# Kernel tuning notes

Hardware: AMD Instinct MI355X
Metric: run time of the kernel (lower is better)

The kernel has to match this reference:

```python
import jax, jax.numpy as jnp
import numpy as np

B, NC, P, HW, ED = 64, 20, 4, 224, 128  # batch, num_classes, patch, img, embed_dim
LN_EPS = 1e-5


def setup_inputs() -> dict:
    key = jax.random.key(0)
    k0, k1, k2, k3 = jax.random.split(key, 4)
    rgb = jax.random.normal(k0, (B, 3, HW, HW), jnp.float32)
    mask = jax.random.randint(k1, (B, 1, HW, HW), 0, NC).astype(jnp.int32)
    proj_w = jax.random.normal(k2, (ED, 4, P, P), jnp.float32) * 0.05  # OIHW, in=3+1
    proj_b = jnp.zeros((ED,), jnp.float32)
    ln_gamma = jnp.ones((ED,), jnp.float32)
    ln_beta = jnp.zeros((ED,), jnp.float32)
    sem_emb = jax.random.normal(k3, (NC, ED), jnp.float32) * 0.02
    # weights_dict = {3: 2.0, 7: 5.0, 15: 3.0} on top of ones
    class_weights = jnp.ones((NC,), jnp.float32).at[jnp.array([3, 7, 15])].set(
        jnp.array([2.0, 5.0, 3.0], jnp.float32))
    return dict(rgb=rgb, mask=mask, proj_w=proj_w, proj_b=proj_b,
                ln_gamma=ln_gamma, ln_beta=ln_beta, sem_emb=sem_emb,
                class_weights=class_weights)


def reference(rgb, mask, proj_w, proj_b, ln_gamma, ln_beta, sem_emb, class_weights):
    Bsz, _, H, W = rgb.shape
    Hp, Wp = H // P, W // P
    # --- patch conv embed on [rgb ; mask] ---
    x = jnp.concatenate([rgb, mask.astype(rgb.dtype)], axis=1)  # [B,4,H,W]
    pt = jax.lax.conv_general_dilated(
        x, proj_w, window_strides=(P, P), padding='VALID',
        dimension_numbers=('NCHW', 'OIHW', 'NCHW'))  # [B,ED,Hp,Wp]
    pt = pt + proj_b[None, :, None, None]
    pt = pt.reshape(Bsz, ED, Hp * Wp).transpose(0, 2, 1)  # [B,N,ED]
    # --- LayerNorm over embed dim ---
    mu = pt.mean(-1, keepdims=True)
    var = ((pt - mu) ** 2).mean(-1, keepdims=True)
    pt = (pt - mu) / jnp.sqrt(var + LN_EPS) * ln_gamma + ln_beta
    # --- importance-weighted area histogram downsample (no big one-hot) ---
    m = mask[:, 0].astype(jnp.int32)  # [B,H,W]
    patches = m.reshape(Bsz, Hp, P, Wp, P).transpose(0, 1, 3, 2, 4)
    patches = patches.reshape(Bsz, Hp, Wp, P * P)  # [B,Hp,Wp,16] pixel labels per patch
    # per-patch class counts; fixed small loop over NC classes
    counts = jnp.stack([(patches == c).sum(-1) for c in range(NC)], axis=-1)
    score = counts.astype(jnp.float32) * class_weights  # [B,Hp,Wp,NC]
    down_mask = jnp.argmax(score, axis=-1)  # [B,Hp,Wp]
    # --- semantic embedding add ---
    sem = sem_emb[down_mask.reshape(Bsz, -1)]  # [B,N,ED]
    out = (pt + sem).reshape(Bsz, Hp, Wp, ED)
    return out, (Hp, Wp)
```

## Files before the change

kernel.cpp:

```cpp
#include <hip/hip_runtime.h>

#define HWD 224
#define NPP 3136
#define WPD 56
#define EDIM 128
#define NCLS 20
#define NPATCH 200704
#define NOUT (NPATCH*EDIM)
#define TPW 8
#define NBLK (NPATCH/(16*TPW))

typedef float  f32x4  __attribute__((ext_vector_type(4)));
typedef int    i32x4  __attribute__((ext_vector_type(4)));
typedef __bf16 bf16x8 __attribute__((ext_vector_type(8)));

static __device__ __forceinline__ unsigned bfpair(float a, float b) {
    unsigned ua = __float_as_uint(a), ub = __float_as_uint(b);
    ua = (ua + 0x7fffu + ((ua >> 16) & 1u)) >> 16;
    ub = (ub + 0x7fffu + ((ub >> 16) & 1u)) & 0xffff0000u;
    return ua | ub;
}
static __device__ __forceinline__ bf16x8 pack8(float4 lo, float4 hi) {
    i32x4 v;
    v.x = bfpair(lo.x, lo.y); v.y = bfpair(lo.z, lo.w);
    v.z = bfpair(hi.x, hi.y); v.w = bfpair(hi.z, hi.w);
    return __builtin_bit_cast(bf16x8, v);
}

__global__ __launch_bounds__(64)
__attribute__((amdgpu_waves_per_eu(2, 2)))
void fused_patch_embed_mfma(
    const float* __restrict__ rgb, const int* __restrict__ mask,
    const float* __restrict__ wgt, const float* __restrict__ pb,
    const float* __restrict__ gam, const float* __restrict__ bet,
    const float* __restrict__ sem, const float* __restrict__ cw,
    float* __restrict__ out, int out_size)
{
    const int lane = (int)threadIdx.x;
    const int g  = lane >> 4;
    const int n0 = lane & 15;

    bf16x8 bw[8][2];
#pragma unroll
    for (int t = 0; t < 8; ++t) {
        const float* wr = wgt + (size_t)(t * 16 + n0) * 64;
#pragma unroll
        for (int ks = 0; ks < 2; ++ks) {
            const float4 lo = *(const float4*)(wr + ks * 32 + g * 8);
            const float4 hi = *(const float4*)(wr + ks * 32 + g * 8 + 4);
            bw[t][ks] = pack8(lo, hi);
        }
    }
    float gam_l[8], bet_l[8], pb_l[8];
#pragma unroll
    for (int t = 0; t < 8; ++t) {
        gam_l[t] = gam[t * 16 + n0];
        bet_l[t] = bet[t * 16 + n0];
        pb_l[t]  = pb[t * 16 + n0];
    }

    const int ch0 = g >> 1;
    const int kh0 = (g & 1) * 2;

    const int tile0 = (int)blockIdx.x * TPW;
    for (int ti = 0; ti < TPW; ++ti) {
        const int tile = tile0 + ti;
        const int p  = tile * 16 + n0;
        const int b  = p / NPP;
        const int r  = p - b * NPP;
        const int hp = r / WPD;
        const int wp = r - hp * WPD;
        const int rowpix = hp * 4 + kh0;

        const float* rb0 = rgb + ((size_t)(b * 3 + ch0) * HWD + rowpix) * HWD + wp * 4;
        const float4 x0 = *(const float4*)(rb0);
        const float4 x1 = *(const float4*)(rb0 + HWD);
        const float* rb2 = rgb + ((size_t)(b * 3 + 2) * HWD + rowpix) * HWD + wp * 4;
        const int*   mb  = mask + ((size_t)b * HWD + rowpix) * HWD + wp * 4;
        const int* src1 = (g < 2) ? (const int*)rb2 : mb;
        const int4 y0i = *(const int4*)(src1);
        const int4 y1i = *(const int4*)(src1 + HWD);
        float4 y0, y1;
        if (g < 2) {
            y0 = make_float4(__int_as_float(y0i.x), __int_as_float(y0i.y),
                             __int_as_float(y0i.z), __int_as_float(y0i.w));
            y1 = make_float4(__int_as_float(y1i.x), __int_as_float(y1i.y),
                             __int_as_float(y1i.z), __int_as_float(y1i.w));
        } else {
            y0 = make_float4((float)y0i.x, (float)y0i.y, (float)y0i.z, (float)y0i.w);
            y1 = make_float4((float)y1i.x, (float)y1i.y, (float)y1i.z, (float)y1i.w);
        }
        const bf16x8 a0 = pack8(x0, x1);
        const bf16x8 a1 = pack8(y0, y1);

        f32x4 acc[8];
#pragma unroll
        for (int t = 0; t < 8; ++t) {
            f32x4 c; c[0] = c[1] = c[2] = c[3] = pb_l[t];
            c = __builtin_amdgcn_mfma_f32_16x16x32_bf16(a0, bw[t][0], c, 0, 0, 0);
            acc[t] = __builtin_amdgcn_mfma_f32_16x16x32_bf16(a1, bw[t][1], c, 0, 0, 0);
        }

        float s[4], q[4];
#pragma unroll
        for (int rr = 0; rr < 4; ++rr) {
            float ss = 0.f, qq = 0.f;
#pragma unroll
            for (int t = 0; t < 8; ++t) { const float v = acc[t][rr]; ss += v; qq = fmaf(v, v, qq); }
            s[rr] = ss; q[rr] = qq;
        }
#pragma unroll
        for (int m = 8; m >= 1; m >>= 1) {
#pragma unroll
            for (int rr = 0; rr < 4; ++rr) {
                s[rr] += __shfl_xor(s[rr], m, 64);
                q[rr] += __shfl_xor(q[rr], m, 64);
            }
        }
        float mu[4], rs[4];
#pragma unroll
        for (int rr = 0; rr < 4; ++rr) {
            mu[rr] = s[rr] * (1.f / EDIM);
            rs[rr] = rsqrtf(q[rr] * (1.f / EDIM) - mu[rr] * mu[rr] + 1e-5f);
        }

        unsigned pk0 = 0, pk1 = 0, pk2 = 0, pk3 = 0;
#define CNT1(val) { const unsigned v = (unsigned)(val) & 31u;                 \
                    const unsigned qw = (v * 43u) >> 8;                       \
                    const unsigned bit = 1u << (5u * (v - 6u * qw));          \
                    pk0 += (qw == 0u) ? bit : 0u; pk1 += (qw == 1u) ? bit : 0u; \
                    pk2 += (qw == 2u) ? bit : 0u; pk3 += (qw == 3u) ? bit : 0u; }
        CNT1(y0i.x) CNT1(y0i.y) CNT1(y0i.z) CNT1(y0i.w)
        CNT1(y1i.x) CNT1(y1i.y) CNT1(y1i.z) CNT1(y1i.w)
#undef CNT1
        pk0 += __shfl_xor(pk0, 16, 64); pk1 += __shfl_xor(pk1, 16, 64);
        pk2 += __shfl_xor(pk2, 16, 64); pk3 += __shfl_xor(pk3, 16, 64);

        float bs = -1.f; int best = 0;
#pragma unroll
        for (int c = 0; c < NCLS; ++c) {
            const unsigned word = (c < 6) ? pk0 : (c < 12) ? pk1 : (c < 18) ? pk2 : pk3;
            const unsigned cnt = (word >> (5 * (c % 6))) & 31u;
            const float sc = (float)cnt * cw[c];
            if (sc > bs) { bs = sc; best = c; }
        }
        int bestr[4];
#pragma unroll
        for (int rr = 0; rr < 4; ++rr)
            bestr[rr] = __shfl(best, 32 + g * 4 + rr, 64);

#pragma unroll
        for (int rr = 0; rr < 4; ++rr) {
            const int pm = tile * 16 + g * 4 + rr;
            float* op = out + (size_t)pm * EDIM + n0;
            const float* sr = sem + (size_t)bestr[rr] * EDIM + n0;
#pragma unroll
            for (int t = 0; t < 8; ++t) {
                op[t * 16] = fmaf((acc[t][rr] - mu[rr]) * rs[rr], gam_l[t], bet_l[t]) + sr[t * 16];
            }
        }
    }

    if (blockIdx.x == 0 && lane == 0) {
        for (int i = NOUT; i < out_size; ++i) out[i] = 56.0f;
    }
}

extern "C" void kernel_launch(void* const* d_in, const int* in_sizes, int n_in,
                              void* d_out, int out_size, void* d_ws, size_t ws_size,
                              hipStream_t stream) {
    const float* rgb  = (const float*)d_in[0];
    const int*   mask = (const int*)d_in[1];
    const float* wgt  = (const float*)d_in[2];
    const float* pb   = (const float*)d_in[3];
    const float* gam  = (const float*)d_in[4];
    const float* bet  = (const float*)d_in[5];
    const float* sem  = (const float*)d_in[6];
    const float* cw   = (const float*)d_in[7];
    float* out = (float*)d_out;

    fused_patch_embed_mfma<<<NBLK, 64, 0, stream>>>(rgb, mask, wgt, pb, gam, bet,
                                                    sem, cw, out, out_size);
}
```

Before: 172.0 us.

## Switch to 32x32x16 MFMA with transposed layout, prefetch and float4 stores

Moves from 16x16x32 MFMA with patches as the A operand to 32x32x16 MFMA, where the weights are the A operand and 32 patches form the B columns. Each lane now owns one patch's pixel data and a run of output channels, so the LayerNorm reduction needs a single cross-half shuffle and outputs are written as float4 rows. Loads for the next tile are software-prefetched into a double buffer. The aim is to cut shuffle and scalar-store overhead and to hide load latency. In exchange it uses more registers per lane (16-wide accumulators and prefetch buffers) and reloads gamma, beta and bias from memory inside the loop.

```diff
diff --git a/kernel.cpp b/kernel.cpp
--- a/kernel.cpp
+++ b/kernel.cpp
@@ -7,10 +7,10 @@
 #define NCLS 20
 #define NPATCH 200704
 #define NOUT (NPATCH*EDIM)
-#define TPW 8
-#define NBLK (NPATCH/(16*TPW))
+#define TPW 4
+#define NBLK (NPATCH/(32*TPW))
 
-typedef float  f32x4  __attribute__((ext_vector_type(4)));
+typedef float  f32x16 __attribute__((ext_vector_type(16)));
 typedef int    i32x4  __attribute__((ext_vector_type(4)));
 typedef __bf16 bf16x8 __attribute__((ext_vector_type(8)));
 
@@ -27,9 +27,33 @@
     return __builtin_bit_cast(bf16x8, v);
 }
 
+struct Pix { float4 r[6]; i32x4 m[2]; int p; };
+
+static __device__ __forceinline__ Pix load_pix(const float* __restrict__ rgb,
+                                               const int* __restrict__ mask,
+                                               int tile, int pt, int hi) {
+    Pix o;
+    o.p = tile * 32 + pt;
+    const int b  = o.p / NPP;
+    const int r  = o.p - b * NPP;
+    const int hp = r / WPD;
+    const int wp = r - hp * WPD;
+    const int row = hp * 4 + hi * 2;
+    const float* base = rgb + ((size_t)(b * 3) * HWD + row) * HWD + wp * 4;
+#pragma unroll
+    for (int s = 0; s < 3; ++s) {
+        o.r[2*s]   = *(const float4*)(base + (size_t)s * HWD * HWD);
+        o.r[2*s+1] = *(const float4*)(base + (size_t)s * HWD * HWD + HWD);
+    }
+    const int* mb = mask + ((size_t)b * HWD + row) * HWD + wp * 4;
+    o.m[0] = *(const i32x4*)(mb);
+    o.m[1] = *(const i32x4*)(mb + HWD);
+    return o;
+}
+
 __global__ __launch_bounds__(64)
 __attribute__((amdgpu_waves_per_eu(2, 2)))
-void fused_patch_embed_mfma(
+void fused_patch_embed_mfma32(
     const float* __restrict__ rgb, const int* __restrict__ mask,
     const float* __restrict__ wgt, const float* __restrict__ pb,
     const float* __restrict__ gam, const float* __restrict__ bet,
@@ -37,126 +61,103 @@
     float* __restrict__ out, int out_size)
 {
     const int lane = (int)threadIdx.x;
-    const int g  = lane >> 4;
-    const int n0 = lane & 15;
+    const int pt = lane & 31;
+    const int hi = lane >> 5;
 
-    bf16x8 bw[8][2];
+    bf16x8 aw[4][4];
 #pragma unroll
-    for (int t = 0; t < 8; ++t) {
-        const float* wr = wgt + (size_t)(t * 16 + n0) * 64;
+    for (int t = 0; t < 4; ++t) {
 #pragma unroll
-        for (int ks = 0; ks < 2; ++ks) {
-            const float4 lo = *(const float4*)(wr + ks * 32 + g * 8);
-            const float4 hi = *(const float4*)(wr + ks * 32 + g * 8 + 4);
-            bw[t][ks] = pack8(lo, hi);
+        for (int s = 0; s < 4; ++s) {
+            const float* wr = wgt + (size_t)(t * 32 + pt) * 64 + s * 16 + hi * 8;
+            aw[t][s] = pack8(*(const float4*)wr, *(const float4*)(wr + 4));
         }
     }
-    float gam_l[8], bet_l[8], pb_l[8];
+    float cwv[NCLS];
 #pragma unroll
-    for (int t = 0; t < 8; ++t) {
-        gam_l[t] = gam[t * 16 + n0];
-        bet_l[t] = bet[t * 16 + n0];
-        pb_l[t]  = pb[t * 16 + n0];
-    }
-
-    const int ch0 = g >> 1;
-    const int kh0 = (g & 1) * 2;
+    for (int c = 0; c < NCLS; ++c) cwv[c] = cw[c];
 
     const int tile0 = (int)blockIdx.x * TPW;
+    Pix px[2];
+    px[0] = load_pix(rgb, mask, tile0, pt, hi);
+
+#pragma unroll
     for (int ti = 0; ti < TPW; ++ti) {
-        const int tile = tile0 + ti;
-        const int p  = tile * 16 + n0;
-        const int b  = p / NPP;
-        const int r  = p - b * NPP;
-        const int hp = r / WPD;
-        const int wp = r - hp * WPD;
-        const int rowpix = hp * 4 + kh0;
+        if (ti + 1 < TPW)
+            px[(ti + 1) & 1] = load_pix(rgb, mask, tile0 + ti + 1, pt, hi);
+        const Pix c = px[ti & 1];
 
-        const float* rb0 = rgb + ((size_t)(b * 3 + ch0) * HWD + rowpix) * HWD + wp * 4;
-        const float4 x0 = *(const float4*)(rb0);
-        const float4 x1 = *(const float4*)(rb0 + HWD);
-        const float* rb2 = rgb + ((size_t)(b * 3 + 2) * HWD + rowpix) * HWD + wp * 4;
-        const int*   mb  = mask + ((size_t)b * HWD + rowpix) * HWD + wp * 4;
-        const int* src1 = (g < 2) ? (const int*)rb2 : mb;
-        const int4 y0i = *(const int4*)(src1);
-        const int4 y1i = *(const int4*)(src1 + HWD);
-        float4 y0, y1;
-        if (g < 2) {
-            y0 = make_float4(__int_as_float(y0i.x), __int_as_float(y0i.y),
-                             __int_as_float(y0i.z), __int_as_float(y0i.w));
-            y1 = make_float4(__int_as_float(y1i.x), __int_as_float(y1i.y),
-                             __int_as_float(y1i.z), __int_as_float(y1i.w));
-        } else {
-            y0 = make_float4((float)y0i.x, (float)y0i.y, (float)y0i.z, (float)y0i.w);
-            y1 = make_float4((float)y1i.x, (float)y1i.y, (float)y1i.z, (float)y1i.w);
-        }
-        const bf16x8 a0 = pack8(x0, x1);
-        const bf16x8 a1 = pack8(y0, y1);
+        bf16x8 bx[4];
+        bx[0] = pack8(c.r[0], c.r[1]);
+        bx[1] = pack8(c.r[2], c.r[3]);
+        bx[2] = pack8(c.r[4], c.r[5]);
+        const float4 mf0 = make_float4((float)c.m[0].x, (float)c.m[0].y,
+                                       (float)c.m[0].z, (float)c.m[0].w);
+        const float4 mf1 = make_float4((float)c.m[1].x, (float)c.m[1].y,
+                                       (float)c.m[1].z, (float)c.m[1].w);
+        bx[3] = pack8(mf0, mf1);
 
-        f32x4 acc[8];
+        f32x16 acc[4];
 #pragma unroll
-        for (int t = 0; t < 8; ++t) {
-            f32x4 c; c[0] = c[1] = c[2] = c[3] = pb_l[t];
-            c = __builtin_amdgcn_mfma_f32_16x16x32_bf16(a0, bw[t][0], c, 0, 0, 0);
-            acc[t] = __builtin_amdgcn_mfma_f32_16x16x32_bf16(a1, bw[t][1], c, 0, 0, 0);
+        for (int t = 0; t < 4; ++t) {
+            f32x16 a;
+#pragma unroll
+            for (int q = 0; q < 4; ++q) {
+                const float4 pv = *(const float4*)(pb + t * 32 + 8 * q + 4 * hi);
+                a[4*q+0] = pv.x; a[4*q+1] = pv.y; a[4*q+2] = pv.z; a[4*q+3] = pv.w;
+            }
+#pragma unroll
+            for (int s = 0; s < 4; ++s)
+                a = __builtin_amdgcn_mfma_f32_32x32x16_bf16(aw[t][s], bx[s], a, 0, 0, 0);
+            acc[t] = a;
         }
 
-        float s[4], q[4];
+        float ss = 0.f, qq = 0.f;
 #pragma unroll
-        for (int rr = 0; rr < 4; ++rr) {
-            float ss = 0.f, qq = 0.f;
+        for (int t = 0; t < 4; ++t)
 #pragma unroll
-            for (int t = 0; t < 8; ++t) { const float v = acc[t][rr]; ss += v; qq = fmaf(v, v, qq); }
-            s[rr] = ss; q[rr] = qq;
-        }
+            for (int e = 0; e < 16; ++e) { const float v = acc[t][e]; ss += v; qq = fmaf(v, v, qq); }
+        ss += __shfl_xor(ss, 32, 64);
+        qq += __shfl_xor(qq, 32, 64);
+        const float mu   = ss * (1.f / EDIM);
+        const float rstd = rsqrtf(qq * (1.f / EDIM) - mu * mu + 1e-5f);
+
+        unsigned pk0 = 0, pk1 = 0, pk2 = 0, pk3 = 0;
+#define CNT1(val) { const unsigned v = (unsigned)(val) & 31u;                   \
+                    const unsigned qw = (v * 43u) >> 8;                         \
+                    const unsigned bit = 1u << (5u * (v - 6u * qw));            \
+                    pk0 += (qw == 0u) ? bit : 0u; pk1 += (qw == 1u) ? bit : 0u; \
+                    pk2 += (qw == 2u) ? bit : 0u; pk3 += (qw == 3u) ? bit : 0u; }
+        CNT1(c.m[0].x) CNT1(c.m[0].y) CNT1(c.m[0].z) CNT1(c.m[0].w)
+        CNT1(c.m[1].x) CNT1(c.m[1].y) CNT1(c.m[1].z) CNT1(c.m[1].w)
+#undef CNT1
+        pk0 += __shfl_xor(pk0, 32, 64); pk1 += __shfl_xor(pk1, 32, 64);
+        pk2 += __shfl_xor(pk2, 32, 64); pk3 += __shfl_xor(pk3, 32, 64);
+        float bs = -1.f; int best = 0;
 #pragma unroll
-        for (int m = 8; m >= 1; m >>= 1) {
-#pragma unroll
-            for (int rr = 0; rr < 4; ++rr) {
-                s[rr] += __shfl_xor(s[rr], m, 64);
-                q[rr] += __shfl_xor(q[rr], m, 64);
-            }
-        }
-        float mu[4], rs[4];
-#pragma unroll
-        for (int rr = 0; rr < 4; ++rr) {
-            mu[rr] = s[rr] * (1.f / EDIM);
-            rs[rr] = rsqrtf(q[rr] * (1.f / EDIM) - mu[rr] * mu[rr] + 1e-5f);
+        for (int cc = 0; cc < NCLS; ++cc) {
+            const unsigned word = (cc < 6) ? pk0 : (cc < 12) ? pk1 : (cc < 18) ? pk2 : pk3;
+            const unsigned cnt = (word >> (5 * (cc % 6))) & 31u;
+            const float sc = (float)cnt * cwv[cc];
+            if (sc > bs) { bs = sc; best = cc; }
         }
 
-        unsigned pk0 = 0, pk1 = 0, pk2 = 0, pk3 = 0;
-#define CNT1(val) { const unsigned v = (unsigned)(val) & 31u;                 \
-                    const unsigned qw = (v * 43u) >> 8;                       \
-                    const unsigned bit = 1u << (5u * (v - 6u * qw));          \
-                    pk0 += (qw == 0u) ? bit : 0u; pk1 += (qw == 1u) ? bit : 0u; \
-                    pk2 += (qw == 2u) ? bit : 0u; pk3 += (qw == 3u) ? bit : 0u; }
-        CNT1(y0i.x) CNT1(y0i.y) CNT1(y0i.z) CNT1(y0i.w)
-        CNT1(y1i.x) CNT1(y1i.y) CNT1(y1i.z) CNT1(y1i.w)
-#undef CNT1
-        pk0 += __shfl_xor(pk0, 16, 64); pk1 += __shfl_xor(pk1, 16, 64);
-        pk2 += __shfl_xor(pk2, 16, 64); pk3 += __shfl_xor(pk3, 16, 64);
-
-        float bs = -1.f; int best = 0;
+        const float* sr = sem + (size_t)best * EDIM + 4 * hi;
+        float* op = out + (size_t)c.p * EDIM + 4 * hi;
 #pragma unroll
-        for (int c = 0; c < NCLS; ++c) {
-            const unsigned word = (c < 6) ? pk0 : (c < 12) ? pk1 : (c < 18) ? pk2 : pk3;
-            const unsigned cnt = (word >> (5 * (c % 6))) & 31u;
-            const float sc = (float)cnt * cw[c];
-            if (sc > bs) { bs = sc; best = c; }
-        }
-        int bestr[4];
+        for (int t = 0; t < 4; ++t) {
 #pragma unroll
-        for (int rr = 0; rr < 4; ++rr)
-            bestr[rr] = __shfl(best, 32 + g * 4 + rr, 64);
-
-#pragma unroll
-        for (int rr = 0; rr < 4; ++rr) {
-            const int pm = tile * 16 + g * 4 + rr;
-            float* op = out + (size_t)pm * EDIM + n0;
-            const float* sr = sem + (size_t)bestr[rr] * EDIM + n0;
-#pragma unroll
-            for (int t = 0; t < 8; ++t) {
-                op[t * 16] = fmaf((acc[t][rr] - mu[rr]) * rs[rr], gam_l[t], bet_l[t]) + sr[t * 16];
+            for (int q = 0; q < 4; ++q) {
+                const int off = t * 32 + 8 * q;
+                const float4 g4 = *(const float4*)(gam + off + 4 * hi);
+                const float4 b4 = *(const float4*)(bet + off + 4 * hi);
+                const float4 s4 = *(const float4*)(sr + off);
+                float4 o;
+                o.x = fmaf((acc[t][4*q+0] - mu) * rstd, g4.x, b4.x) + s4.x;
+                o.y = fmaf((acc[t][4*q+1] - mu) * rstd, g4.y, b4.y) + s4.y;
+                o.z = fmaf((acc[t][4*q+2] - mu) * rstd, g4.z, b4.z) + s4.z;
+                o.w = fmaf((acc[t][4*q+3] - mu) * rstd, g4.w, b4.w) + s4.w;
+                *(float4*)(op + off) = o;
             }
         }
     }
@@ -179,6 +180,6 @@
     const float* cw   = (const float*)d_in[7];
     float* out = (float*)d_out;
 
-    fused_patch_embed_mfma<<<NBLK, 64, 0, stream>>>(rgb, mask, wgt, pb, gam, bet,
-                                                    sem, cw, out, out_size);
+    fused_patch_embed_mfma32<<<NBLK, 64, 0, stream>>>(rgb, mask, wgt, pb, gam, bet,
+                                                      sem, cw, out, out_size);
 }
```

New measurement: 274.3 us. 1.59x slower.
